# Optimization experiments

Hardware: AMD Instinct MI355X
Metric: run time of the kernel (lower is better)

## Reference

```python
import jax, jax.numpy as jnp
import numpy as np

ENT_TOTAL = 1_000_000
REL_TOTAL = 10_000
HIDDEN = 128      # == ent_size == rel_size
REL_TYPE = 1_000
MARGIN = 1.0
BATCH = 8192


def setup_inputs() -> dict:
    key = jax.random.key(0)
    ks = jax.random.split(key, 10)
    return {
        "ent_emb": jax.random.normal(ks[0], (ENT_TOTAL, HIDDEN), jnp.float32) * 0.05,
        "rel_emb": jax.random.normal(ks[1], (REL_TOTAL, HIDDEN), jnp.float32) * 0.05,
        "type_mat": jax.random.normal(ks[2], (REL_TYPE, HIDDEN * HIDDEN), jnp.float32) * 0.05,
        "pos_h": jax.random.randint(ks[3], (BATCH,), 0, ENT_TOTAL, jnp.int64 if jax.config.jax_enable_x64 else jnp.int32),
        "pos_t": jax.random.randint(ks[4], (BATCH,), 0, ENT_TOTAL, jnp.int32),
        "pos_r": jax.random.randint(ks[5], (BATCH,), 0, REL_TOTAL, jnp.int32),
        "pos_type_r": jax.random.randint(ks[6], (BATCH,), 0, REL_TYPE, jnp.int32),
        "neg_h": jax.random.randint(ks[7], (BATCH,), 0, ENT_TOTAL, jnp.int32),
        "neg_t": jax.random.randint(ks[8], (BATCH,), 0, ENT_TOTAL, jnp.int32),
        "neg_r": jax.random.randint(ks[9], (BATCH,), 0, REL_TOTAL, jnp.int32),
    }


def _l2norm(x):
    return x * jax.lax.rsqrt(jnp.sum(x * x, axis=-1, keepdims=True) + 1e-12)


def _calc(h, t, r):
    # l2-normalize each, then |h + r - t|
    return jnp.abs(_l2norm(h) + _l2norm(r) - _l2norm(t))


def reference(ent_emb, rel_emb, type_mat, pos_h, pos_t, pos_r, pos_type_r,
              neg_h, neg_t, neg_r):
    B = pos_h.shape[0]
    D = ent_emb.shape[1]
    # gathers
    p_h = ent_emb[pos_h]                       # [B, D]
    p_t = ent_emb[pos_t]
    p_r = rel_emb[pos_r]
    n_h = ent_emb[neg_h]
    n_t = ent_emb[neg_t]
    n_r = rel_emb[neg_r]
    # per-sample transfer matrix; original code uses pos_type_r for BOTH
    # positive and negative (faithful to source).
    T = type_mat[pos_type_r].reshape(B, D, D)  # [B, ent_size, rel_size]
    # per-sample transfer: [B, D] x [B, D, R] -> [B, R]
    p_h_ = jnp.einsum('bd,bdr->br', p_h, T)
    p_t_ = jnp.einsum('bd,bdr->br', p_t, T)
    n_h_ = jnp.einsum('bd,bdr->br', n_h, T)
    n_t_ = jnp.einsum('bd,bdr->br', n_t, T)
    p_score = jnp.sum(_calc(p_h_, p_t_, p_r), axis=-1, keepdims=True)  # [B,1]
    n_score = jnp.sum(_calc(n_h_, n_t_, n_r), axis=-1, keepdims=True)
    loss = jnp.mean(jnp.maximum(p_score - n_score + MARGIN, 0.0))
    return loss
```

## Files before the change

### kernel.cpp

```cpp
#include <hip/hip_runtime.h>

#define D 128
#define CHUNK 64
#define NW 4
#define MAX_TYPES 1024
#define MAX_B 8192
#define MARGIN 1.0f

#define WS_NITEMS 0
#define WS_ORDER  64
#define WS_ITEMS  8448
#define WS_NEEDED ((size_t)(WS_ITEMS + 4 * 2048) * 4)


__global__ __launch_bounds__(1024) void group_kernel(
    const int* __restrict__ type_r, int* __restrict__ ws,
    float* __restrict__ out, int B, int ntype)
{
    __shared__ int hist[MAX_TYPES];
    __shared__ int typec[MAX_B];
    __shared__ int wsum[16], wsum2[16];
    const int tid = threadIdx.x;
    const int lane = tid & 63;
    const int wv = tid >> 6;

    if (tid == 0) out[0] = 0.0f;
    hist[tid] = 0;
    __syncthreads();

    const int B4 = B >> 2;
    const int4* t4p = (const int4*)type_r;
    for (int i = tid; i < B4; i += 1024) {
        const int4 t = t4p[i];
        typec[i * 4 + 0] = t.x; atomicAdd(&hist[t.x], 1);
        typec[i * 4 + 1] = t.y; atomicAdd(&hist[t.y], 1);
        typec[i * 4 + 2] = t.z; atomicAdd(&hist[t.z], 1);
        typec[i * 4 + 3] = t.w; atomicAdd(&hist[t.w], 1);
    }
    for (int i = (B4 << 2) + tid; i < B; i += 1024) {
        const int t = type_r[i];
        typec[i] = t;
        atomicAdd(&hist[t], 1);
    }
    __syncthreads();

    const int c  = (tid < ntype) ? hist[tid] : 0;
    const int ic = (c + CHUNK - 1) / CHUNK;
    int vc = c, vic = ic;
    #pragma unroll
    for (int off = 1; off < 64; off <<= 1) {
        const int tc  = __shfl_up(vc,  off);
        const int tic = __shfl_up(vic, off);
        if (lane >= off) { vc += tc; vic += tic; }
    }
    if (lane == 63) { wsum[wv] = vc; wsum2[wv] = vic; }
    __syncthreads();
    if (wv == 0 && lane < 16) {
        int a = wsum[lane], b = wsum2[lane];
        #pragma unroll
        for (int off = 1; off < 16; off <<= 1) {
            const int ta = __shfl_up(a, off);
            const int tb = __shfl_up(b, off);
            if (lane >= off) { a += ta; b += tb; }
        }
        wsum[lane] = a; wsum2[lane] = b;
    }
    __syncthreads();
    const int base_c  = (wv ? wsum[wv - 1]  : 0) + vc - c;
    const int base_ic = (wv ? wsum2[wv - 1] : 0) + vic - ic;
    hist[tid] = base_c;
    if (tid < ntype && ic > 0) {
        int4* items = (int4*)(ws + WS_ITEMS);
        for (int k = 0; k < ic; ++k)
            items[base_ic + k] = make_int4(tid, base_c + k * CHUNK,
                                           min(CHUNK, c - k * CHUNK), 0);
    }
    if (tid == 0) ws[WS_NITEMS] = wsum2[15];
    __syncthreads();
    for (int i = tid; i < B; i += 1024) {
        const int p = atomicAdd(&hist[typec[i]], 1);
        ws[WS_ORDER + p] = i;
    }
}


#define BFLY5(x) { x += __shfl_xor(x, 1); x += __shfl_xor(x, 2); x += __shfl_xor(x, 4); \
                   x += __shfl_xor(x, 8); x += __shfl_xor(x, 16); }

#define FMA4(A, T, S) { (A).x = fmaf((T).x, (S), (A).x); (A).y = fmaf((T).y, (S), (A).y); \
                        (A).z = fmaf((T).z, (S), (A).z); (A).w = fmaf((T).w, (S), (A).w); }

struct SampleRegs {
    float2 e0, e1, e2, e3;
    float4 rp, rn;
};

__device__ __forceinline__ void fetch_sample(
    SampleRegs& S, int o,
    const float* __restrict__ ent, const float* __restrict__ rel,
    const int* __restrict__ pos_h, const int* __restrict__ pos_t,
    const int* __restrict__ pos_r, const int* __restrict__ neg_h,
    const int* __restrict__ neg_t, const int* __restrict__ neg_r,
    int l, int cg)
{
    const size_t b0 = (size_t)pos_h[o] * D;
    const size_t b1 = (size_t)pos_t[o] * D;
    const size_t b2 = (size_t)neg_h[o] * D;
    const size_t b3 = (size_t)neg_t[o] * D;
    const size_t r0 = (size_t)pos_r[o] * D;
    const size_t r1 = (size_t)neg_r[o] * D;
    S.e0 = *(const float2*)&ent[b0 + 2 * l];
    S.e1 = *(const float2*)&ent[b1 + 2 * l];
    S.e2 = *(const float2*)&ent[b2 + 2 * l];
    S.e3 = *(const float2*)&ent[b3 + 2 * l];
    S.rp = *(const float4*)&rel[r0 + 4 * cg];
    S.rn = *(const float4*)&rel[r1 + 4 * cg];
}

__device__ __forceinline__ void commit_sample(float* vbs, const SampleRegs& S, int l) {
    *(float2*)&vbs[0 * D + 2 * l] = S.e0;
    *(float2*)&vbs[1 * D + 2 * l] = S.e1;
    *(float2*)&vbs[2 * D + 2 * l] = S.e2;
    *(float2*)&vbs[3 * D + 2 * l] = S.e3;
}

__device__ __forceinline__ float sscore(const float4 a[4], float4 rp, float4 rn) {
    float sph = a[0].x*a[0].x + a[0].y*a[0].y + a[0].z*a[0].z + a[0].w*a[0].w;
    float spt = a[1].x*a[1].x + a[1].y*a[1].y + a[1].z*a[1].z + a[1].w*a[1].w;
    float snh = a[2].x*a[2].x + a[2].y*a[2].y + a[2].z*a[2].z + a[2].w*a[2].w;
    float snt = a[3].x*a[3].x + a[3].y*a[3].y + a[3].z*a[3].z + a[3].w*a[3].w;
    float spr = rp.x*rp.x + rp.y*rp.y + rp.z*rp.z + rp.w*rp.w;
    float snr = rn.x*rn.x + rn.y*rn.y + rn.z*rn.z + rn.w*rn.w;
    BFLY5(sph); BFLY5(spt); BFLY5(snh); BFLY5(snt); BFLY5(spr); BFLY5(snr);
    const float iph = rsqrtf(sph + 1e-12f);
    const float ipt = rsqrtf(spt + 1e-12f);
    const float inh = rsqrtf(snh + 1e-12f);
    const float itn = rsqrtf(snt + 1e-12f);
    const float ipr = rsqrtf(spr + 1e-12f);
    const float inr = rsqrtf(snr + 1e-12f);
    float z = fabsf(a[0].x*iph + rp.x*ipr - a[1].x*ipt)
            + fabsf(a[0].y*iph + rp.y*ipr - a[1].y*ipt)
            + fabsf(a[0].z*iph + rp.z*ipr - a[1].z*ipt)
            + fabsf(a[0].w*iph + rp.w*ipr - a[1].w*ipt)
            - fabsf(a[2].x*inh + rn.x*inr - a[3].x*itn)
            - fabsf(a[2].y*inh + rn.y*inr - a[3].y*itn)
            - fabsf(a[2].z*inh + rn.z*inr - a[3].z*itn)
            - fabsf(a[2].w*inh + rn.w*inr - a[3].w*itn);
    BFLY5(z);
    return fmaxf(z + MARGIN, 0.f);
}

__device__ __forceinline__ void pair_score(
    const float* __restrict__ T_lds, const float* __restrict__ vbw,
    const SampleRegs& A, const SampleRegs& Bq,
    int h, int cg, bool hasB, float& wl)
{
    const float4* __restrict__ T4 = (const float4*)T_lds;
    const float4* __restrict__ vA = (const float4*)vbw;
    const float4* __restrict__ vB = vA + 128;
    float4 aA[4], aB[4];
    #pragma unroll
    for (int r = 0; r < 4; ++r) {
        aA[r] = make_float4(0.f, 0.f, 0.f, 0.f);
        aB[r] = make_float4(0.f, 0.f, 0.f, 0.f);
    }
    const int rb = h * 64;
    const int vb0 = h * 16;
    #pragma unroll 4
    for (int dg = 0; dg < 16; ++dg) {
        const int row = rb + dg * 4;
        const float4 t0 = T4[(row + 0) * 32 + cg];
        const float4 t1 = T4[(row + 1) * 32 + cg];
        const float4 t2 = T4[(row + 2) * 32 + cg];
        const float4 t3 = T4[(row + 3) * 32 + cg];
        const int vi = vb0 + dg;
        #pragma unroll
        for (int r = 0; r < 4; ++r) {
            const float4 va = vA[r * 32 + vi];
            FMA4(aA[r], t0, va.x); FMA4(aA[r], t1, va.y);
            FMA4(aA[r], t2, va.z); FMA4(aA[r], t3, va.w);
            const float4 vbv = vB[r * 32 + vi];
            FMA4(aB[r], t0, vbv.x); FMA4(aB[r], t1, vbv.y);
            FMA4(aB[r], t2, vbv.z); FMA4(aB[r], t3, vbv.w);
        }
    }
    #pragma unroll
    for (int r = 0; r < 4; ++r) {
        aA[r].x += __shfl_xor(aA[r].x, 32); aA[r].y += __shfl_xor(aA[r].y, 32);
        aA[r].z += __shfl_xor(aA[r].z, 32); aA[r].w += __shfl_xor(aA[r].w, 32);
        aB[r].x += __shfl_xor(aB[r].x, 32); aB[r].y += __shfl_xor(aB[r].y, 32);
        aB[r].z += __shfl_xor(aB[r].z, 32); aB[r].w += __shfl_xor(aB[r].w, 32);
    }
    wl += sscore(aA, A.rp, A.rn);
    if (hasB) wl += sscore(aB, Bq.rp, Bq.rn);
}

__global__ __launch_bounds__(256, 2) void fused_kernel(
    const float* __restrict__ ent,
    const float* __restrict__ rel,
    const float* __restrict__ tmat,
    const int* __restrict__ pos_h,
    const int* __restrict__ pos_t,
    const int* __restrict__ pos_r,
    const int* __restrict__ neg_h,
    const int* __restrict__ neg_t,
    const int* __restrict__ neg_r,
    const int* __restrict__ ws,
    float* __restrict__ out,
    float inv_B)
{
    const int nit = ws[WS_NITEMS];
    if (blockIdx.x >= nit) return;
    const int4 item = ((const int4*)(ws + WS_ITEMS))[blockIdx.x];
    const int type  = item.x;
    const int start = item.y;
    const int cnt   = item.z;

    const int tid = threadIdx.x;
    const int l   = tid & 63;
    const int w   = tid >> 6;
    const int cg  = l & 31;
    const int h   = l >> 5;

    __shared__ float T_lds[D * D];
    __shared__ float vbuf[NW][2][4][D];

    {
        const float4* Tg = (const float4*)(tmat + (size_t)type * (D * D));
        float4* Ts = (float4*)T_lds;
        #pragma unroll
        for (int k = 0; k < 16; ++k)
            Ts[tid + k * 256] = Tg[tid + k * 256];
    }
    __syncthreads();

    const int* ordr = ws + WS_ORDER;
    float* vbw = &vbuf[w][0][0][0];

    float wl = 0.f;
    int ja = w;
    if (ja < cnt) {
        SampleRegs A0, A1, B0, B1;
        int jb = (ja + NW < cnt) ? ja + NW : ja;
        bool curHasB = (jb != ja);
        fetch_sample(A0, ordr[start + ja], ent, rel, pos_h, pos_t, pos_r,
                     neg_h, neg_t, neg_r, l, cg);
        fetch_sample(A1, ordr[start + jb], ent, rel, pos_h, pos_t, pos_r,
                     neg_h, neg_t, neg_r, l, cg);
        for (;;) {
            commit_sample(vbw,          A0, l);
            commit_sample(vbw + 4 * D,  A1, l);
            const int jn = ja + 2 * NW;
            const bool more = jn < cnt;
            bool nextHasB = false;
            if (more) {
                const int jnb = (jn + NW < cnt) ? jn + NW : jn;
                nextHasB = (jnb != jn);
                fetch_sample(B0, ordr[start + jn], ent, rel, pos_h, pos_t, pos_r,
                             neg_h, neg_t, neg_r, l, cg);
                fetch_sample(B1, ordr[start + jnb], ent, rel, pos_h, pos_t, pos_r,
                             neg_h, neg_t, neg_r, l, cg);
            }
            pair_score(T_lds, vbw, A0, A1, h, cg, curHasB, wl);
            if (!more) break;
            ja = jn; A0 = B0; A1 = B1; curHasB = nextHasB;
        }
    }

    if (l == 0) vbuf[w][0][0][0] = wl;
    __syncthreads();
    if (tid == 0) {
        float s = 0.f;
        #pragma unroll
        for (int k = 0; k < NW; ++k) s += vbuf[k][0][0][0];
        atomicAdd(out, s * inv_B);
    }
}


__global__ __launch_bounds__(128) void transr_fallback(
    const float* __restrict__ ent, const float* __restrict__ rel,
    const float* __restrict__ tmat,
    const int* __restrict__ pos_h, const int* __restrict__ pos_t,
    const int* __restrict__ pos_r, const int* __restrict__ pos_type_r,
    const int* __restrict__ neg_h, const int* __restrict__ neg_t,
    const int* __restrict__ neg_r, float* __restrict__ out, int B)
{
    const int b = blockIdx.x;
    const int r = threadIdx.x;
    const int lane = r & 63;
    const int wid = r >> 6;
    __shared__ float4 vcomb[D];
    __shared__ float sred[16];
    vcomb[r] = make_float4(ent[(size_t)pos_h[b]*D + r], ent[(size_t)pos_t[b]*D + r],
                           ent[(size_t)neg_h[b]*D + r], ent[(size_t)neg_t[b]*D + r]);
    const float prr = rel[(size_t)pos_r[b] * D + r];
    const float nrr = rel[(size_t)neg_r[b] * D + r];
    __syncthreads();
    const float* __restrict__ T = tmat + (size_t)pos_type_r[b] * (D * D);
    float aph = 0.f, apt = 0.f, anh = 0.f, ant = 0.f;
    #pragma unroll 8
    for (int d = 0; d < D; ++d) {
        const float t = T[d * D + r];
        const float4 v = vcomb[d];
        aph = fmaf(v.x, t, aph); apt = fmaf(v.y, t, apt);
        anh = fmaf(v.z, t, anh); ant = fmaf(v.w, t, ant);
    }
    float s0 = aph*aph, s1 = apt*apt, s2 = anh*anh, s3 = ant*ant;
    float s4 = prr*prr, s5 = nrr*nrr;
    #pragma unroll
    for (int off = 32; off; off >>= 1) {
        s0 += __shfl_xor(s0, off); s1 += __shfl_xor(s1, off);
        s2 += __shfl_xor(s2, off); s3 += __shfl_xor(s3, off);
        s4 += __shfl_xor(s4, off); s5 += __shfl_xor(s5, off);
    }
    if (lane == 0) {
        sred[wid*8+0]=s0; sred[wid*8+1]=s1; sred[wid*8+2]=s2;
        sred[wid*8+3]=s3; sred[wid*8+4]=s4; sred[wid*8+5]=s5;
    }
    __syncthreads();
    const float iph = rsqrtf(sred[0]+sred[8] +1e-12f);
    const float ipt = rsqrtf(sred[1]+sred[9] +1e-12f);
    const float inh = rsqrtf(sred[2]+sred[10]+1e-12f);
    const float itn = rsqrtf(sred[3]+sred[11]+1e-12f);
    const float ipr = rsqrtf(sred[4]+sred[12]+1e-12f);
    const float inr = rsqrtf(sred[5]+sred[13]+1e-12f);
    float pterm = fabsf(aph*iph + prr*ipr - apt*ipt);
    float nterm = fabsf(anh*inh + nrr*inr - ant*itn);
    #pragma unroll
    for (int off = 32; off; off >>= 1) {
        pterm += __shfl_xor(pterm, off);
        nterm += __shfl_xor(nterm, off);
    }
    __syncthreads();
    if (lane == 0) { sred[wid*2+0] = pterm; sred[wid*2+1] = nterm; }
    __syncthreads();
    if (r == 0)
        atomicAdd(out, fmaxf(sred[0]+sred[2] - sred[1]-sred[3] + MARGIN, 0.f) / (float)B);
}


extern "C" void kernel_launch(void* const* d_in, const int* in_sizes, int n_in,
                              void* d_out, int out_size, void* d_ws, size_t ws_size,
                              hipStream_t stream) {
    const float* ent  = (const float*)d_in[0];
    const float* rel  = (const float*)d_in[1];
    const float* tmat = (const float*)d_in[2];
    const int* pos_h      = (const int*)d_in[3];
    const int* pos_t      = (const int*)d_in[4];
    const int* pos_r      = (const int*)d_in[5];
    const int* pos_type_r = (const int*)d_in[6];
    const int* neg_h      = (const int*)d_in[7];
    const int* neg_t      = (const int*)d_in[8];
    const int* neg_r      = (const int*)d_in[9];
    float* out = (float*)d_out;
    const int B = in_sizes[3];
    const int ntype = in_sizes[2] / (D * D);

    if (ws_size < WS_NEEDED || ntype > MAX_TYPES || B > MAX_B) {
        hipMemsetAsync(out, 0, sizeof(float), stream);
        transr_fallback<<<B, 128, 0, stream>>>(
            ent, rel, tmat, pos_h, pos_t, pos_r, pos_type_r,
            neg_h, neg_t, neg_r, out, B);
        return;
    }

    int* ws = (int*)d_ws;
    group_kernel<<<1, 1024, 0, stream>>>(pos_type_r, ws, out, B, ntype);
    fused_kernel<<<1280, 256, 0, stream>>>(
        ent, rel, tmat, pos_h, pos_t, pos_r, neg_h, neg_t, neg_r,
        ws, out, 1.0f / (float)B);
}
```

Baseline: 57.55 us.

## Use 8 waves per block with one sample per wave and early gather prefetch

New measurement: 48.05 us. 16.5% less time.

```diff
diff --git a/kernel.cpp b/kernel.cpp
--- a/kernel.cpp
+++ b/kernel.cpp
@@ -2,7 +2,6 @@
 
 #define D 128
 #define CHUNK 64
-#define NW 4
 #define MAX_TYPES 1024
 #define MAX_B 8192
 #define MARGIN 1.0f
@@ -117,18 +116,52 @@
     S.rn = *(const float4*)&rel[r1 + 4 * cg];
 }
 
-__device__ __forceinline__ void commit_sample(float* vbs, const SampleRegs& S, int l) {
-    *(float2*)&vbs[0 * D + 2 * l] = S.e0;
-    *(float2*)&vbs[1 * D + 2 * l] = S.e1;
-    *(float2*)&vbs[2 * D + 2 * l] = S.e2;
-    *(float2*)&vbs[3 * D + 2 * l] = S.e3;
-}
-
-__device__ __forceinline__ float sscore(const float4 a[4], float4 rp, float4 rn) {
-    float sph = a[0].x*a[0].x + a[0].y*a[0].y + a[0].z*a[0].z + a[0].w*a[0].w;
-    float spt = a[1].x*a[1].x + a[1].y*a[1].y + a[1].z*a[1].z + a[1].w*a[1].w;
-    float snh = a[2].x*a[2].x + a[2].y*a[2].y + a[2].z*a[2].z + a[2].w*a[2].w;
-    float snt = a[3].x*a[3].x + a[3].y*a[3].y + a[3].z*a[3].z + a[3].w*a[3].w;
+__device__ __forceinline__ void commit_sample(float* vbw, const SampleRegs& S, int l) {
+    *(float2*)&vbw[0 * D + 2 * l] = S.e0;
+    *(float2*)&vbw[1 * D + 2 * l] = S.e1;
+    *(float2*)&vbw[2 * D + 2 * l] = S.e2;
+    *(float2*)&vbw[3 * D + 2 * l] = S.e3;
+}
+
+__device__ __forceinline__ float sample_score(
+    const float* __restrict__ T_lds, const float* __restrict__ vbw,
+    int h, int cg, float4 rp, float4 rn)
+{
+    const float4* __restrict__ T4 = (const float4*)T_lds;
+    const float4* __restrict__ vv = (const float4*)vbw;
+    float4 a0 = make_float4(0.f, 0.f, 0.f, 0.f), a1 = a0, a2 = a0, a3 = a0;
+    const int rb  = h * 64;
+    const int vb0 = h * 16;
+    #pragma unroll 4
+    for (int dg = 0; dg < 16; ++dg) {
+        const int row = rb + dg * 4;
+        const float4 t0 = T4[(row + 0) * 32 + cg];
+        const float4 t1 = T4[(row + 1) * 32 + cg];
+        const float4 t2 = T4[(row + 2) * 32 + cg];
+        const float4 t3 = T4[(row + 3) * 32 + cg];
+        const int vi = vb0 + dg;
+        const float4 v0 = vv[0 * 32 + vi];
+        FMA4(a0, t0, v0.x); FMA4(a0, t1, v0.y); FMA4(a0, t2, v0.z); FMA4(a0, t3, v0.w);
+        const float4 v1 = vv[1 * 32 + vi];
+        FMA4(a1, t0, v1.x); FMA4(a1, t1, v1.y); FMA4(a1, t2, v1.z); FMA4(a1, t3, v1.w);
+        const float4 v2 = vv[2 * 32 + vi];
+        FMA4(a2, t0, v2.x); FMA4(a2, t1, v2.y); FMA4(a2, t2, v2.z); FMA4(a2, t3, v2.w);
+        const float4 v3 = vv[3 * 32 + vi];
+        FMA4(a3, t0, v3.x); FMA4(a3, t1, v3.y); FMA4(a3, t2, v3.z); FMA4(a3, t3, v3.w);
+    }
+    a0.x += __shfl_xor(a0.x, 32); a0.y += __shfl_xor(a0.y, 32);
+    a0.z += __shfl_xor(a0.z, 32); a0.w += __shfl_xor(a0.w, 32);
+    a1.x += __shfl_xor(a1.x, 32); a1.y += __shfl_xor(a1.y, 32);
+    a1.z += __shfl_xor(a1.z, 32); a1.w += __shfl_xor(a1.w, 32);
+    a2.x += __shfl_xor(a2.x, 32); a2.y += __shfl_xor(a2.y, 32);
+    a2.z += __shfl_xor(a2.z, 32); a2.w += __shfl_xor(a2.w, 32);
+    a3.x += __shfl_xor(a3.x, 32); a3.y += __shfl_xor(a3.y, 32);
+    a3.z += __shfl_xor(a3.z, 32); a3.w += __shfl_xor(a3.w, 32);
+
+    float sph = a0.x*a0.x + a0.y*a0.y + a0.z*a0.z + a0.w*a0.w;
+    float spt = a1.x*a1.x + a1.y*a1.y + a1.z*a1.z + a1.w*a1.w;
+    float snh = a2.x*a2.x + a2.y*a2.y + a2.z*a2.z + a2.w*a2.w;
+    float snt = a3.x*a3.x + a3.y*a3.y + a3.z*a3.z + a3.w*a3.w;
     float spr = rp.x*rp.x + rp.y*rp.y + rp.z*rp.z + rp.w*rp.w;
     float snr = rn.x*rn.x + rn.y*rn.y + rn.z*rn.z + rn.w*rn.w;
     BFLY5(sph); BFLY5(spt); BFLY5(snh); BFLY5(snt); BFLY5(spr); BFLY5(snr);
@@ -138,64 +171,19 @@
     const float itn = rsqrtf(snt + 1e-12f);
     const float ipr = rsqrtf(spr + 1e-12f);
     const float inr = rsqrtf(snr + 1e-12f);
-    float z = fabsf(a[0].x*iph + rp.x*ipr - a[1].x*ipt)
-            + fabsf(a[0].y*iph + rp.y*ipr - a[1].y*ipt)
-            + fabsf(a[0].z*iph + rp.z*ipr - a[1].z*ipt)
-            + fabsf(a[0].w*iph + rp.w*ipr - a[1].w*ipt)
-            - fabsf(a[2].x*inh + rn.x*inr - a[3].x*itn)
-            - fabsf(a[2].y*inh + rn.y*inr - a[3].y*itn)
-            - fabsf(a[2].z*inh + rn.z*inr - a[3].z*itn)
-            - fabsf(a[2].w*inh + rn.w*inr - a[3].w*itn);
+    float z = fabsf(a0.x*iph + rp.x*ipr - a1.x*ipt)
+            + fabsf(a0.y*iph + rp.y*ipr - a1.y*ipt)
+            + fabsf(a0.z*iph + rp.z*ipr - a1.z*ipt)
+            + fabsf(a0.w*iph + rp.w*ipr - a1.w*ipt)
+            - fabsf(a2.x*inh + rn.x*inr - a3.x*itn)
+            - fabsf(a2.y*inh + rn.y*inr - a3.y*itn)
+            - fabsf(a2.z*inh + rn.z*inr - a3.z*itn)
+            - fabsf(a2.w*inh + rn.w*inr - a3.w*itn);
     BFLY5(z);
     return fmaxf(z + MARGIN, 0.f);
 }
 
-__device__ __forceinline__ void pair_score(
-    const float* __restrict__ T_lds, const float* __restrict__ vbw,
-    const SampleRegs& A, const SampleRegs& Bq,
-    int h, int cg, bool hasB, float& wl)
-{
-    const float4* __restrict__ T4 = (const float4*)T_lds;
-    const float4* __restrict__ vA = (const float4*)vbw;
-    const float4* __restrict__ vB = vA + 128;
-    float4 aA[4], aB[4];
-    #pragma unroll
-    for (int r = 0; r < 4; ++r) {
-        aA[r] = make_float4(0.f, 0.f, 0.f, 0.f);
-        aB[r] = make_float4(0.f, 0.f, 0.f, 0.f);
-    }
-    const int rb = h * 64;
-    const int vb0 = h * 16;
-    #pragma unroll 4
-    for (int dg = 0; dg < 16; ++dg) {
-        const int row = rb + dg * 4;
-        const float4 t0 = T4[(row + 0) * 32 + cg];
-        const float4 t1 = T4[(row + 1) * 32 + cg];
-        const float4 t2 = T4[(row + 2) * 32 + cg];
-        const float4 t3 = T4[(row + 3) * 32 + cg];
-        const int vi = vb0 + dg;
-        #pragma unroll
-        for (int r = 0; r < 4; ++r) {
-            const float4 va = vA[r * 32 + vi];
-            FMA4(aA[r], t0, va.x); FMA4(aA[r], t1, va.y);
-            FMA4(aA[r], t2, va.z); FMA4(aA[r], t3, va.w);
-            const float4 vbv = vB[r * 32 + vi];
-            FMA4(aB[r], t0, vbv.x); FMA4(aB[r], t1, vbv.y);
-            FMA4(aB[r], t2, vbv.z); FMA4(aB[r], t3, vbv.w);
-        }
-    }
-    #pragma unroll
-    for (int r = 0; r < 4; ++r) {
-        aA[r].x += __shfl_xor(aA[r].x, 32); aA[r].y += __shfl_xor(aA[r].y, 32);
-        aA[r].z += __shfl_xor(aA[r].z, 32); aA[r].w += __shfl_xor(aA[r].w, 32);
-        aB[r].x += __shfl_xor(aB[r].x, 32); aB[r].y += __shfl_xor(aB[r].y, 32);
-        aB[r].z += __shfl_xor(aB[r].z, 32); aB[r].w += __shfl_xor(aB[r].w, 32);
-    }
-    wl += sscore(aA, A.rp, A.rn);
-    if (hasB) wl += sscore(aB, Bq.rp, Bq.rn);
-}
-
-__global__ __launch_bounds__(256, 2) void fused_kernel(
+__global__ __launch_bounds__(512, 4) void fused_kernel(
     const float* __restrict__ ent,
     const float* __restrict__ rel,
     const float* __restrict__ tmat,
@@ -223,56 +211,49 @@
     const int h   = l >> 5;
 
     __shared__ float T_lds[D * D];
-    __shared__ float vbuf[NW][2][4][D];
+    __shared__ float vbuf[8][4][D];
+
+    const int* ordr = ws + WS_ORDER;
+
+    SampleRegs A, Bq;
+    int j = w;
+    const bool active = (j < cnt);
+    if (active)
+        fetch_sample(A, ordr[start + j], ent, rel, pos_h, pos_t, pos_r,
+                     neg_h, neg_t, neg_r, l, cg);
 
     {
         const float4* Tg = (const float4*)(tmat + (size_t)type * (D * D));
         float4* Ts = (float4*)T_lds;
         #pragma unroll
-        for (int k = 0; k < 16; ++k)
-            Ts[tid + k * 256] = Tg[tid + k * 256];
-    }
-    __syncthreads();
-
-    const int* ordr = ws + WS_ORDER;
-    float* vbw = &vbuf[w][0][0][0];
-
+        for (int k = 0; k < 8; ++k)
+            Ts[tid + k * 512] = Tg[tid + k * 512];
+    }
+    __syncthreads();
+
+    float* vbw = &vbuf[w][0][0];
     float wl = 0.f;
-    int ja = w;
-    if (ja < cnt) {
-        SampleRegs A0, A1, B0, B1;
-        int jb = (ja + NW < cnt) ? ja + NW : ja;
-        bool curHasB = (jb != ja);
-        fetch_sample(A0, ordr[start + ja], ent, rel, pos_h, pos_t, pos_r,
-                     neg_h, neg_t, neg_r, l, cg);
-        fetch_sample(A1, ordr[start + jb], ent, rel, pos_h, pos_t, pos_r,
-                     neg_h, neg_t, neg_r, l, cg);
+
+    if (active) {
         for (;;) {
-            commit_sample(vbw,          A0, l);
-            commit_sample(vbw + 4 * D,  A1, l);
-            const int jn = ja + 2 * NW;
+            commit_sample(vbw, A, l);
+            const int jn = j + 8;
             const bool more = jn < cnt;
-            bool nextHasB = false;
-            if (more) {
-                const int jnb = (jn + NW < cnt) ? jn + NW : jn;
-                nextHasB = (jnb != jn);
-                fetch_sample(B0, ordr[start + jn], ent, rel, pos_h, pos_t, pos_r,
+            if (more)
+                fetch_sample(Bq, ordr[start + jn], ent, rel, pos_h, pos_t, pos_r,
                              neg_h, neg_t, neg_r, l, cg);
-                fetch_sample(B1, ordr[start + jnb], ent, rel, pos_h, pos_t, pos_r,
-                             neg_h, neg_t, neg_r, l, cg);
-            }
-            pair_score(T_lds, vbw, A0, A1, h, cg, curHasB, wl);
+            wl += sample_score(T_lds, vbw, h, cg, A.rp, A.rn);
             if (!more) break;
-            ja = jn; A0 = B0; A1 = B1; curHasB = nextHasB;
+            j = jn; A = Bq;
         }
     }
 
-    if (l == 0) vbuf[w][0][0][0] = wl;
+    if (l == 0) vbuf[w][0][0] = wl;
     __syncthreads();
     if (tid == 0) {
         float s = 0.f;
         #pragma unroll
-        for (int k = 0; k < NW; ++k) s += vbuf[k][0][0][0];
+        for (int k = 0; k < 8; ++k) s += vbuf[k][0][0];
         atomicAdd(out, s * inv_B);
     }
 }
@@ -367,7 +348,7 @@
 
     int* ws = (int*)d_ws;
     group_kernel<<<1, 1024, 0, stream>>>(pos_type_r, ws, out, B, ntype);
-    fused_kernel<<<1280, 256, 0, stream>>>(
+    fused_kernel<<<1280, 512, 0, stream>>>(
         ent, rel, tmat, pos_h, pos_t, pos_r, neg_h, neg_t, neg_r,
         ws, out, 1.0f / (float)B);
 }
```
